# Kernel tuning notes

Hardware: AMD Instinct MI355X
Metric: run time of the kernel (lower is better)

## Reference

```python
import jax, jax.numpy as jnp
import numpy as np

B, F, D = 1024, 39, 16
HIDDEN = [128, 128, 128]


def _cin(x, Ws, bs):
    # x: (B, F0, D) stacked field embeddings
    F0 = x.shape[1]
    h = x  # hidden_nn_layers[-1], shape (B, Fk, D)
    outs = []
    n = len(Ws)
    for i, (W, b) in enumerate(zip(Ws, bs)):
        L = W.shape[-1]
        Fk = h.shape[1]
        Wr = W.reshape(F0, Fk, L)  # conv1d kernel [1, F0*Fk, L] -> (F0, Fk, L)
        # per-embedding-dim field outer product: (B, F0, Fk, D)
        z = jnp.einsum('bfd,bgd->bfgd', x, h)
        # pointwise conv over D + bias + relu -> (B, L, D)
        cur = jax.nn.relu(jnp.einsum('bfgd,fgl->bld', z, Wr) + b[None, :, None])
        if i != n - 1:
            h = cur[:, : L // 2]          # next_hidden
            direct = cur[:, L // 2 :]     # direct_connect
        else:
            direct = cur
        outs.append(direct)
    # concat over field axis, sum over embedding dim -> (B, sum_direct)
    return jnp.concatenate(outs, axis=1).sum(-1)


def setup_inputs() -> dict:
    key = jax.random.key(0)
    ks = jax.random.split(key, 8)
    x = jax.random.normal(ks[0], (B, F, D), dtype=jnp.float32)
    field_nums = [F]
    Ws, bs = [], []
    for i, L in enumerate(HIDDEN):
        fan_in = field_nums[0] * field_nums[-1]
        lim = np.sqrt(6.0 / fan_in)  # he_uniform
        Ws.append(jax.random.uniform(ks[1 + i], (fan_in, L), jnp.float32, -lim, lim))
        bs.append(jnp.zeros((L,), jnp.float32))
        field_nums.append(L // 2)
    return {"x": x, "W0": Ws[0], "W1": Ws[1], "W2": Ws[2],
            "b0": bs[0], "b1": bs[1], "b2": bs[2]}


def reference(x, W0, W1, W2, b0, b1, b2):
    return _cin(x, [W0, W1, W2], [b0, b1, b2])
```

## Files before the change

kernel.cpp:

```cpp
#include <hip/hip_runtime.h>


#define NF     39
#define LCH    128
#define NLAYER 3

typedef __bf16        bf16x8 __attribute__((ext_vector_type(8)));
typedef unsigned int  uint4v __attribute__((ext_vector_type(4)));
typedef float         f32x4  __attribute__((ext_vector_type(4)));
typedef float         f32x8  __attribute__((ext_vector_type(8)));

__device__ __forceinline__ unsigned short f2bf_rne(float f) {
    unsigned u = __float_as_uint(f);
    u += 0x7fffu + ((u >> 16) & 1u);
    return (unsigned short)(u >> 16);
}

#define PACKBF(SRC) __builtin_bit_cast(bf16x8, (uint4v){                                             \
    __builtin_amdgcn_perm(__float_as_uint((SRC)[1]), __float_as_uint((SRC)[0]), 0x07060302u),        \
    __builtin_amdgcn_perm(__float_as_uint((SRC)[3]), __float_as_uint((SRC)[2]), 0x07060302u),        \
    __builtin_amdgcn_perm(__float_as_uint((SRC)[5]), __float_as_uint((SRC)[4]), 0x07060302u),        \
    __builtin_amdgcn_perm(__float_as_uint((SRC)[7]), __float_as_uint((SRC)[6]), 0x07060302u)})

#define LOADW(DA, DB, L, FO)                                                   \
  do { int _pl = (L), _pf = (FO);                                              \
    if (_pf >= NF) { _pf -= NF; ++_pl; }                                       \
    if (_pl < NLAYER) {                                                        \
      const float* _base = (_pl == 0) ? (W0 + _pf * 4992)                      \
                         : (_pl == 1) ? (W1 + _pf * 8192)                      \
                                      : (W2 + _pf * 8192);                     \
      const float* _p0 = _base + lane_off;                                     \
      DA[0] = _p0[0];   DA[1] = _p0[128]; DA[2] = _p0[256]; DA[3] = _p0[384];  \
      DA[4] = _p0[512]; DA[5] = _p0[640]; DA[6] = _p0[768]; DA[7] = _p0[896];  \
      if (_pl == 0) {                                                          \
        if (q == 0) {                                                          \
          const float* _p1 = _base + 4096 + nc;                                \
          DB[0] = _p1[0];   DB[1] = _p1[128]; DB[2] = _p1[256];                \
          DB[3] = _p1[384]; DB[4] = _p1[512]; DB[5] = _p1[640];                \
          DB[6] = _p1[768]; DB[7] = 0.f;                                       \
        } else { DB = (f32x8){0,0,0,0,0,0,0,0}; }                              \
      } else {                                                                 \
        const float* _p1 = _p0 + 4096;                                         \
        DB[0] = _p1[0];   DB[1] = _p1[128]; DB[2] = _p1[256]; DB[3] = _p1[384];\
        DB[4] = _p1[512]; DB[5] = _p1[640]; DB[6] = _p1[768]; DB[7] = _p1[896];\
      }                                                                        \
    }                                                                          \
  } while (0)

__device__ __forceinline__ void mfma_step(
    const bf16x8 a00, const bf16x8 a01, const bf16x8 a02, const bf16x8 a03,
    const bf16x8 a10, const bf16x8 a11, const bf16x8 a12, const bf16x8 a13,
    const f32x8& ra, const f32x8& rb,
    f32x4& cur0, f32x4& cur1, f32x4& cur2, f32x4& cur3,
    const float* xrow, int q)
{
    const bf16x8 B0 = PACKBF(ra);
    const bf16x8 B1 = PACKBF(rb);
    const f32x4 z = {0.f, 0.f, 0.f, 0.f};
    f32x4 s0 = __builtin_amdgcn_mfma_f32_16x16x32_bf16(a00, B0, z, 0, 0, 0);
    f32x4 s1 = __builtin_amdgcn_mfma_f32_16x16x32_bf16(a01, B0, z, 0, 0, 0);
    f32x4 s2 = __builtin_amdgcn_mfma_f32_16x16x32_bf16(a02, B0, z, 0, 0, 0);
    f32x4 s3 = __builtin_amdgcn_mfma_f32_16x16x32_bf16(a03, B0, z, 0, 0, 0);
    s0 = __builtin_amdgcn_mfma_f32_16x16x32_bf16(a10, B1, s0, 0, 0, 0);
    s1 = __builtin_amdgcn_mfma_f32_16x16x32_bf16(a11, B1, s1, 0, 0, 0);
    s2 = __builtin_amdgcn_mfma_f32_16x16x32_bf16(a12, B1, s2, 0, 0, 0);
    s3 = __builtin_amdgcn_mfma_f32_16x16x32_bf16(a13, B1, s3, 0, 0, 0);
    const f32x4 xr0 = *(const f32x4*)&xrow[ 0 + q * 4];
    const f32x4 xr1 = *(const f32x4*)&xrow[16 + q * 4];
    const f32x4 xr2 = *(const f32x4*)&xrow[32 + q * 4];
    const f32x4 xr3 = *(const f32x4*)&xrow[48 + q * 4];
    #pragma unroll
    for (int r = 0; r < 4; ++r) {
        cur0[r] = fmaf(xr0[r], s0[r], cur0[r]);
        cur1[r] = fmaf(xr1[r], s1[r], cur1[r]);
        cur2[r] = fmaf(xr2[r], s2[r], cur2[r]);
        cur3[r] = fmaf(xr3[r], s3[r], cur3[r]);
    }
}

#define HSTORE(CUR, MT)                                                       \
    { hfrag[((nc >> 3) * 64 + (MT) * 16 + q * 4 + 0) * 8 + (nc & 7)] =        \
          f2bf_rne(fmaxf(CUR[0] + bias, 0.f));                                \
      hfrag[((nc >> 3) * 64 + (MT) * 16 + q * 4 + 1) * 8 + (nc & 7)] =        \
          f2bf_rne(fmaxf(CUR[1] + bias, 0.f));                                \
      hfrag[((nc >> 3) * 64 + (MT) * 16 + q * 4 + 2) * 8 + (nc & 7)] =        \
          f2bf_rne(fmaxf(CUR[2] + bias, 0.f));                                \
      hfrag[((nc >> 3) * 64 + (MT) * 16 + q * 4 + 3) * 8 + (nc & 7)] =        \
          f2bf_rne(fmaxf(CUR[3] + bias, 0.f)); }

#define DSTORE(CUR, MT)                                                       \
    { float sacc = fmaxf(CUR[0] + bias, 0.f) + fmaxf(CUR[1] + bias, 0.f)      \
                 + fmaxf(CUR[2] + bias, 0.f) + fmaxf(CUR[3] + bias, 0.f);     \
      sacc += __shfl_xor(sacc, 16, 64);                                       \
      sacc += __shfl_xor(sacc, 32, 64);                                       \
      if (lane < 16) out[(bb + (MT)) * 256 + outcol] = sacc; }

#define LAYERBODY(L, FAa, FAb, FBa, FBb)                                      \
  { const bf16x8 a00 = *(const bf16x8*)&hfrag[((0 + q) * 64 +  0 + c) * 8];   \
    const bf16x8 a01 = *(const bf16x8*)&hfrag[((0 + q) * 64 + 16 + c) * 8];   \
    const bf16x8 a02 = *(const bf16x8*)&hfrag[((0 + q) * 64 + 32 + c) * 8];   \
    const bf16x8 a03 = *(const bf16x8*)&hfrag[((0 + q) * 64 + 48 + c) * 8];   \
    const bf16x8 a10 = *(const bf16x8*)&hfrag[((4 + q) * 64 +  0 + c) * 8];   \
    const bf16x8 a11 = *(const bf16x8*)&hfrag[((4 + q) * 64 + 16 + c) * 8];   \
    const bf16x8 a12 = *(const bf16x8*)&hfrag[((4 + q) * 64 + 32 + c) * 8];   \
    const bf16x8 a13 = *(const bf16x8*)&hfrag[((4 + q) * 64 + 48 + c) * 8];   \
    f32x4 cur0 = {0,0,0,0}, cur1 = {0,0,0,0};                                 \
    f32x4 cur2 = {0,0,0,0}, cur3 = {0,0,0,0};                                 \
    int f = 0;                                                                \
    _Pragma("unroll 1")                                                       \
    for (int it = 0; it < 19; ++it) {                                         \
        mfma_step(a00,a01,a02,a03,a10,a11,a12,a13, FAa, FAb,                  \
                  cur0,cur1,cur2,cur3, &xf32[f * 64], q);                     \
        LOADW(FAa, FAb, (L), f + 2);                                          \
        mfma_step(a00,a01,a02,a03,a10,a11,a12,a13, FBa, FBb,                  \
                  cur0,cur1,cur2,cur3, &xf32[(f + 1) * 64], q);               \
        LOADW(FBa, FBb, (L), f + 3);                                          \
        f += 2;                                                               \
    }                                                                         \
    mfma_step(a00,a01,a02,a03,a10,a11,a12,a13, FAa, FAb,                      \
              cur0,cur1,cur2,cur3, &xf32[38 * 64], q);                        \
    LOADW(FAa, FAb, (L), 40);                                                 \
    const float bias = ((L) == 0) ? biasv0 : ((L) == 1) ? biasv1 : biasv2;    \
    if ((L) < 2 && w < 4) {                                                   \
        HSTORE(cur0, 0) HSTORE(cur1, 1) HSTORE(cur2, 2) HSTORE(cur3, 3)       \
    } else {                                                                  \
        const int outcol = ((L) == 0) ? nc - 64 : ((L) == 1) ? nc : 128 + nc; \
        DSTORE(cur0, 0) DSTORE(cur1, 1) DSTORE(cur2, 2) DSTORE(cur3, 3)       \
    }                                                                         \
    if ((L) < 2) __syncthreads(); }

__global__ __launch_bounds__(512, 1) void cin_mfma(
    const float* __restrict__ x,
    const float* __restrict__ W0,
    const float* __restrict__ W1,
    const float* __restrict__ W2,
    const float* __restrict__ b0p,
    const float* __restrict__ b1p,
    const float* __restrict__ b2p,
    float* __restrict__ out)
{
    __shared__ __align__(16) unsigned short hfrag[8 * 64 * 8];
    __shared__ float xf32[NF * 64];

    const int tid  = threadIdx.x;
    const int lane = tid & 63;
    const int w    = tid >> 6;
    const int q    = lane >> 4;
    const int c    = lane & 15;
    const int nc   = w * 16 + c;
    const int bb   = blockIdx.x * 4;
    const int lane_off = q * 1024 + nc;

    {
        f32x4 zz = {0.f, 0.f, 0.f, 0.f};
        ((f32x4*)hfrag)[tid] = zz;
    }
    __syncthreads();

    for (int i = tid; i < 4 * NF * 16; i += 512) {
        const float v = x[bb * (NF * 16) + i];
        const int lb = i / (NF * 16);
        const int r  = i - lb * (NF * 16);
        const int f  = r >> 4;
        const int d  = r & 15;
        const int sl = lb * 16 + d;
        xf32[f * 64 + sl] = v;
        hfrag[((f >> 3) * 64 + sl) * 8 + (f & 7)] = f2bf_rne(v);
    }
    const float biasv0 = b0p[nc];
    const float biasv1 = b1p[nc];
    const float biasv2 = b2p[nc];

    f32x8 Fa, Fb, Sa, Sb;
    LOADW(Fa, Fb, 0, 0);
    LOADW(Sa, Sb, 0, 1);

    __syncthreads();

    LAYERBODY(0, Fa, Fb, Sa, Sb)
    LAYERBODY(1, Sa, Sb, Fa, Fb)
    LAYERBODY(2, Fa, Fb, Sa, Sb)
}

extern "C" void kernel_launch(void* const* d_in, const int* in_sizes, int n_in,
                              void* d_out, int out_size, void* d_ws, size_t ws_size,
                              hipStream_t stream) {
    const float* x  = (const float*)d_in[0];
    const float* W0 = (const float*)d_in[1];
    const float* W1 = (const float*)d_in[2];
    const float* W2 = (const float*)d_in[3];
    const float* b0 = (const float*)d_in[4];
    const float* b1 = (const float*)d_in[5];
    const float* b2 = (const float*)d_in[6];
    float* out = (float*)d_out;

    cin_mfma<<<256, 512, 0, stream>>>(x, W0, W1, W2, b0, b1, b2, out);
}
```

Baseline: 120.2 us.

## Stagger weight traversal per block and deepen weight prefetch to three stages

Each group of 8 blocks starts the field loop at a different rotated offset, so blocks read different weight slices at the same time instead of all hammering the same addresses. The weight register prefetch deepens from two buffers to three, giving loads more time to arrive before the MFMA step that uses them. The layer loop is now a runtime loop instead of a macro expanded three times, which shrinks code but makes layer selection a runtime branch. The extra modulo index arithmetic and the added register buffers may raise register pressure.

```diff
diff --git a/kernel.cpp b/kernel.cpp
--- a/kernel.cpp
+++ b/kernel.cpp
@@ -22,10 +22,11 @@
     __builtin_amdgcn_perm(__float_as_uint((SRC)[5]), __float_as_uint((SRC)[4]), 0x07060302u),        \
     __builtin_amdgcn_perm(__float_as_uint((SRC)[7]), __float_as_uint((SRC)[6]), 0x07060302u)})
 
-#define LOADW(DA, DB, L, FO)                                                   \
-  do { int _pl = (L), _pf = (FO);                                              \
-    if (_pf >= NF) { _pf -= NF; ++_pl; }                                       \
+#define LOADW(DA, DB, PL_, POS_)                                               \
+  do { int _pl = (PL_), _pp = (POS_);                                          \
+    if (_pp >= NF) { _pp -= NF; ++_pl; }                                       \
     if (_pl < NLAYER) {                                                        \
+      int _pf = _pp + off; if (_pf >= NF) _pf -= NF;                           \
       const float* _base = (_pl == 0) ? (W0 + _pf * 4992)                      \
                          : (_pl == 1) ? (W1 + _pf * 8192)                      \
                                       : (W2 + _pf * 8192);                     \
@@ -95,40 +96,6 @@
       sacc += __shfl_xor(sacc, 32, 64);                                       \
       if (lane < 16) out[(bb + (MT)) * 256 + outcol] = sacc; }
 
-#define LAYERBODY(L, FAa, FAb, FBa, FBb)                                      \
-  { const bf16x8 a00 = *(const bf16x8*)&hfrag[((0 + q) * 64 +  0 + c) * 8];   \
-    const bf16x8 a01 = *(const bf16x8*)&hfrag[((0 + q) * 64 + 16 + c) * 8];   \
-    const bf16x8 a02 = *(const bf16x8*)&hfrag[((0 + q) * 64 + 32 + c) * 8];   \
-    const bf16x8 a03 = *(const bf16x8*)&hfrag[((0 + q) * 64 + 48 + c) * 8];   \
-    const bf16x8 a10 = *(const bf16x8*)&hfrag[((4 + q) * 64 +  0 + c) * 8];   \
-    const bf16x8 a11 = *(const bf16x8*)&hfrag[((4 + q) * 64 + 16 + c) * 8];   \
-    const bf16x8 a12 = *(const bf16x8*)&hfrag[((4 + q) * 64 + 32 + c) * 8];   \
-    const bf16x8 a13 = *(const bf16x8*)&hfrag[((4 + q) * 64 + 48 + c) * 8];   \
-    f32x4 cur0 = {0,0,0,0}, cur1 = {0,0,0,0};                                 \
-    f32x4 cur2 = {0,0,0,0}, cur3 = {0,0,0,0};                                 \
-    int f = 0;                                                                \
-    _Pragma("unroll 1")                                                       \
-    for (int it = 0; it < 19; ++it) {                                         \
-        mfma_step(a00,a01,a02,a03,a10,a11,a12,a13, FAa, FAb,                  \
-                  cur0,cur1,cur2,cur3, &xf32[f * 64], q);                     \
-        LOADW(FAa, FAb, (L), f + 2);                                          \
-        mfma_step(a00,a01,a02,a03,a10,a11,a12,a13, FBa, FBb,                  \
-                  cur0,cur1,cur2,cur3, &xf32[(f + 1) * 64], q);               \
-        LOADW(FBa, FBb, (L), f + 3);                                          \
-        f += 2;                                                               \
-    }                                                                         \
-    mfma_step(a00,a01,a02,a03,a10,a11,a12,a13, FAa, FAb,                      \
-              cur0,cur1,cur2,cur3, &xf32[38 * 64], q);                        \
-    LOADW(FAa, FAb, (L), 40);                                                 \
-    const float bias = ((L) == 0) ? biasv0 : ((L) == 1) ? biasv1 : biasv2;    \
-    if ((L) < 2 && w < 4) {                                                   \
-        HSTORE(cur0, 0) HSTORE(cur1, 1) HSTORE(cur2, 2) HSTORE(cur3, 3)       \
-    } else {                                                                  \
-        const int outcol = ((L) == 0) ? nc - 64 : ((L) == 1) ? nc : 128 + nc; \
-        DSTORE(cur0, 0) DSTORE(cur1, 1) DSTORE(cur2, 2) DSTORE(cur3, 3)       \
-    }                                                                         \
-    if ((L) < 2) __syncthreads(); }
-
 __global__ __launch_bounds__(512, 1) void cin_mfma(
     const float* __restrict__ x,
     const float* __restrict__ W0,
@@ -150,6 +117,7 @@
     const int nc   = w * 16 + c;
     const int bb   = blockIdx.x * 4;
     const int lane_off = q * 1024 + nc;
+    const int off  = (blockIdx.x >> 3) % NF;
 
     {
         f32x4 zz = {0.f, 0.f, 0.f, 0.f};
@@ -171,15 +139,53 @@
     const float biasv1 = b1p[nc];
     const float biasv2 = b2p[nc];
 
-    f32x8 Fa, Fb, Sa, Sb;
-    LOADW(Fa, Fb, 0, 0);
-    LOADW(Sa, Sb, 0, 1);
+    f32x8 P0a, P0b, P1a, P1b, P2a, P2b;
+    LOADW(P0a, P0b, 0, 0);
+    LOADW(P1a, P1b, 0, 1);
+    LOADW(P2a, P2b, 0, 2);
 
     __syncthreads();
 
-    LAYERBODY(0, Fa, Fb, Sa, Sb)
-    LAYERBODY(1, Sa, Sb, Fa, Fb)
-    LAYERBODY(2, Fa, Fb, Sa, Sb)
+    #pragma unroll 1
+    for (int l = 0; l < NLAYER; ++l) {
+        const bf16x8 a00 = *(const bf16x8*)&hfrag[((0 + q) * 64 +  0 + c) * 8];
+        const bf16x8 a01 = *(const bf16x8*)&hfrag[((0 + q) * 64 + 16 + c) * 8];
+        const bf16x8 a02 = *(const bf16x8*)&hfrag[((0 + q) * 64 + 32 + c) * 8];
+        const bf16x8 a03 = *(const bf16x8*)&hfrag[((0 + q) * 64 + 48 + c) * 8];
+        const bf16x8 a10 = *(const bf16x8*)&hfrag[((4 + q) * 64 +  0 + c) * 8];
+        const bf16x8 a11 = *(const bf16x8*)&hfrag[((4 + q) * 64 + 16 + c) * 8];
+        const bf16x8 a12 = *(const bf16x8*)&hfrag[((4 + q) * 64 + 32 + c) * 8];
+        const bf16x8 a13 = *(const bf16x8*)&hfrag[((4 + q) * 64 + 48 + c) * 8];
+
+        f32x4 cur0 = {0,0,0,0}, cur1 = {0,0,0,0};
+        f32x4 cur2 = {0,0,0,0}, cur3 = {0,0,0,0};
+
+        #pragma unroll 1
+        for (int fi = 0; fi < NF; fi += 3) {
+            int f0 = fi + 0 + off; if (f0 >= NF) f0 -= NF;
+            int f1 = fi + 1 + off; if (f1 >= NF) f1 -= NF;
+            int f2 = fi + 2 + off; if (f2 >= NF) f2 -= NF;
+
+            mfma_step(a00,a01,a02,a03,a10,a11,a12,a13, P0a, P0b,
+                      cur0,cur1,cur2,cur3, &xf32[f0 * 64], q);
+            LOADW(P0a, P0b, l, fi + 3);
+            mfma_step(a00,a01,a02,a03,a10,a11,a12,a13, P1a, P1b,
+                      cur0,cur1,cur2,cur3, &xf32[f1 * 64], q);
+            LOADW(P1a, P1b, l, fi + 4);
+            mfma_step(a00,a01,a02,a03,a10,a11,a12,a13, P2a, P2b,
+                      cur0,cur1,cur2,cur3, &xf32[f2 * 64], q);
+            LOADW(P2a, P2b, l, fi + 5);
+        }
+
+        const float bias = (l == 0) ? biasv0 : (l == 1) ? biasv1 : biasv2;
+        if (l < 2 && w < 4) {
+            HSTORE(cur0, 0) HSTORE(cur1, 1) HSTORE(cur2, 2) HSTORE(cur3, 3)
+        } else {
+            const int outcol = (l == 0) ? nc - 64 : (l == 1) ? nc : 128 + nc;
+            DSTORE(cur0, 0) DSTORE(cur1, 1) DSTORE(cur2, 2) DSTORE(cur3, 3)
+        }
+        if (l < 2) __syncthreads();
+    }
 }
 
 extern "C" void kernel_launch(void* const* d_in, const int* in_sizes, int n_in,
```

After: 118.1 us. Within noise of the previous version (-1.7%).
